# Kernel tuning notes

Measured on AMD Instinct MI355X. Metric: run time of the kernel, lower is better.

Reference implementation:

```python
import jax, jax.numpy as jnp
import numpy as np

N_HEADS = 16
D_MODEL = 1024
HEAD_DIM = D_MODEL // N_HEADS
B, S = 2, 2048


def setup_inputs() -> dict:
    key = jax.random.key(0)
    ks = jax.random.split(key, 10)
    scale = 1.0 / np.sqrt(D_MODEL)
    inp = {
        "query_tokens": jax.random.normal(ks[0], (B, S, D_MODEL), dtype=jnp.float32),
        "key_or_value_tokens": jax.random.normal(ks[1], (B, S, D_MODEL), dtype=jnp.float32),
        "mask": jnp.ones((B, S, S), dtype=jnp.int32),
        "Wq": jax.random.normal(ks[2], (D_MODEL, D_MODEL), dtype=jnp.float32) * scale,
        "bq": jnp.zeros((D_MODEL,), dtype=jnp.float32),
        "Wk": jax.random.normal(ks[3], (D_MODEL, D_MODEL), dtype=jnp.float32) * scale,
        "bk": jnp.zeros((D_MODEL,), dtype=jnp.float32),
        "Wv": jax.random.normal(ks[4], (D_MODEL, D_MODEL), dtype=jnp.float32) * scale,
        "bv": jnp.zeros((D_MODEL,), dtype=jnp.float32),
        "Wo": jax.random.normal(ks[5], (D_MODEL, D_MODEL), dtype=jnp.float32) * scale,
        "bo": jnp.zeros((D_MODEL,), dtype=jnp.float32),
    }
    return inp


def reference(query_tokens, key_or_value_tokens, mask, Wq, bq, Wk, bk, Wv, bv, Wo, bo):
    b, s, d = query_tokens.shape
    h, dh = N_HEADS, HEAD_DIM

    def proj(x, W, bias):
        # torch Linear: x @ W.T + b ; then split heads -> (b, h, s, dh)
        y = jnp.einsum("bsd,ed->bse", x, W) + bias
        return y.reshape(b, -1, h, dh).transpose(0, 2, 1, 3)

    q = proj(query_tokens, Wq, bq)
    k = proj(key_or_value_tokens, Wk, bk)
    v = proj(key_or_value_tokens, Wv, bv)

    scores = jnp.einsum("bhqd,bhkd->bhqk", q, k) / jnp.sqrt(jnp.float32(dh))
    # mask: (b, Sq, Sk) -> (b, 1, Sq, Sk); zeros get large negative fill
    scores = jnp.where(mask[:, None, :, :] == 0, jnp.float32(-1e9), scores)
    attn = jax.nn.softmax(scores, axis=-1)
    out = jnp.einsum("bhqk,bhkd->bhqd", attn, v)
    out = out.transpose(0, 2, 1, 3).reshape(b, s, d)
    return jnp.einsum("bsd,ed->bse", out, Wo) + bo
```

## Files before the change

### kernel.cpp

```cpp
#include <hip/hip_runtime.h>
#include <hip/hip_bf16.h>

typedef __bf16 bf16_8  __attribute__((ext_vector_type(8)));
typedef __bf16 bf16_4  __attribute__((ext_vector_type(4)));
typedef float  f32_4   __attribute__((ext_vector_type(4)));

#define NH 16
#define DHD 64
#define BB 2
#define SS 2048
#define DD 1024

__device__ __forceinline__ void gload16(const __bf16* g, __bf16* l) {
    __builtin_amdgcn_global_load_lds(
        (const __attribute__((address_space(1))) void*)g,
        (__attribute__((address_space(3))) void*)l, 16, 0, 0);
}

__global__ __launch_bounds__(256) void conv_mask(
    const float* __restrict__ s0, const float* __restrict__ s1,
    const float* __restrict__ s2, const float* __restrict__ s3,
    const float* __restrict__ s4, const float* __restrict__ s5,
    __bf16* __restrict__ d0, __bf16* __restrict__ d1, __bf16* __restrict__ d2,
    __bf16* __restrict__ d3, __bf16* __restrict__ d4, __bf16* __restrict__ d5,
    const int* __restrict__ mask, int* __restrict__ flags) {
    const int y = blockIdx.y;
    if (y >= 6) {
        if (blockIdx.x >= 1024) return;
        const int id = (y - 6) * 1024 + blockIdx.x;
        const int b = id >> 10, qt = (id >> 5) & 31, kt = id & 31;
        const int t = threadIdx.x;
        const int row = t >> 2, seg = t & 3;
        const int* p = mask + ((size_t)b * SS + qt * 64 + row) * SS + kt * 64 + seg * 16;
        int any0 = 0;
#pragma unroll
        for (int i = 0; i < 4; ++i) {
            int4 v = *(const int4*)&p[i * 4];
            any0 |= (v.x == 0) | (v.y == 0) | (v.z == 0) | (v.w == 0);
        }
        unsigned long long bal = __ballot(any0);
        __shared__ int sf[4];
        if ((t & 63) == 0) sf[t >> 6] = (bal != 0ULL);
        __syncthreads();
        if (t == 0) flags[id] = sf[0] | sf[1] | sf[2] | sf[3];
        return;
    }
    if (y >= 2 && blockIdx.x >= 1024) return;
    const float* s = (y == 0) ? s0 : (y == 1) ? s1 : (y == 2) ? s2
                   : (y == 3) ? s3 : (y == 4) ? s4 : s5;
    __bf16* d      = (y == 0) ? d0 : (y == 1) ? d1 : (y == 2) ? d2
                   : (y == 3) ? d3 : (y == 4) ? d4 : d5;
    const int i = (blockIdx.x * 256 + threadIdx.x) * 4;
    f32_4 v = *(const f32_4*)&s[i];
    bf16_4 o; o[0] = (__bf16)v[0]; o[1] = (__bf16)v[1];
    o[2] = (__bf16)v[2]; o[3] = (__bf16)v[3];
    *(bf16_4*)&d[i] = o;
}

template <int LAYOUT>
__device__ __forceinline__ void gemm_body(const __bf16* __restrict__ A,
                                          const __bf16* __restrict__ W,
                                          const float* __restrict__ bias,
                                          __bf16* __restrict__ out,
                                          __bf16* smem, int m0, int n0) {
    __bf16* ldsA0 = smem;
    __bf16* ldsB0 = smem + 4096;
    __bf16* ldsA1 = smem + 6144;
    __bf16* ldsB1 = smem + 10240;
    __bf16* ldsC  = smem;

    const int tid  = threadIdx.x;
    const int lane = tid & 63;
    const int w    = tid >> 6;
    const int quad = lane >> 4;
    const int l15  = lane & 15;
    const int wm   = w * 32;

    f32_4 acc[2][4] = {};

#define QSTAGE(KT, LA, LB)                                                     \
    do {                                                                       \
        _Pragma("unroll") for (int cc = 0; cc < 2; ++cc) {                     \
            const int c   = tid + cc * 256;                                    \
            const int row = c >> 2;                                            \
            const int cp  = c & 3;                                             \
            gload16(&A[(size_t)(m0 + row) * 1024 + (KT) + cp * 8],             \
                    &(LA)[c * 8]);                                             \
        }                                                                      \
        {                                                                      \
            const int c   = tid;                                               \
            const int row = c >> 2;                                            \
            const int cp  = c & 3;                                             \
            gload16(&W[(size_t)(n0 + row) * 1024 + (KT) + cp * 8],             \
                    &(LB)[c * 8]);                                             \
        }                                                                      \
    } while (0)

    QSTAGE(0, ldsA0, ldsB0);
    __syncthreads();

    for (int kt = 0; kt < 1024; kt += 32) {
        const int sel = (kt >> 5) & 1;
        const __bf16* la = sel ? ldsA1 : ldsA0;
        const __bf16* lb = sel ? ldsB1 : ldsB0;
        __bf16* na       = sel ? ldsA0 : ldsA1;
        __bf16* nb       = sel ? ldsB0 : ldsB1;
        if (kt + 32 < 1024) QSTAGE(kt + 32, na, nb);

        bf16_8 af[2], bfr[4];
#pragma unroll
        for (int i = 0; i < 2; ++i)
            af[i] = *(const bf16_8*)&la[(wm + i * 16 + l15) * 32 + quad * 8];
#pragma unroll
        for (int j = 0; j < 4; ++j)
            bfr[j] = *(const bf16_8*)&lb[(j * 16 + l15) * 32 + quad * 8];
#pragma unroll
        for (int i = 0; i < 2; ++i)
#pragma unroll
            for (int j = 0; j < 4; ++j)
                acc[i][j] = __builtin_amdgcn_mfma_f32_16x16x32_bf16(
                    af[i], bfr[j], acc[i][j], 0, 0, 0);

        __syncthreads();
    }
#undef QSTAGE

    if (LAYOUT == 2) {
#pragma unroll
        for (int i = 0; i < 2; ++i)
#pragma unroll
            for (int j = 0; j < 4; ++j) {
                const int col = n0 + j * 16 + l15;
                const float bv = bias[col];
                bf16_4 pk;
#pragma unroll
                for (int r = 0; r < 4; ++r) pk[r] = (__bf16)(acc[i][j][r] + bv);
                *(bf16_4*)&ldsC[(j * 16 + l15) * 136 + wm + i * 16 + quad * 4] = pk;
            }
        __syncthreads();
#pragma unroll
        for (int it = 0; it < 4; ++it) {
            const int g    = it * 256 + tid;
            const int colp = g >> 4;
            const int s8   = (g & 15) * 8;
            bf16_8 v = *(const bf16_8*)&ldsC[colp * 136 + s8];
            const int gcol = n0 + colp;
            const int grow = m0 + s8;
            *(bf16_8*)&out[(((size_t)(grow >> 11) * NH + (gcol >> 6)) * DHD +
                            (gcol & 63)) * SS + (grow & 2047)] = v;
        }
    } else {
#pragma unroll
        for (int i = 0; i < 2; ++i)
#pragma unroll
            for (int j = 0; j < 4; ++j) {
                const int col = n0 + j * 16 + l15;
                const float bv = bias[col];
#pragma unroll
                for (int r = 0; r < 4; ++r)
                    ldsC[(wm + i * 16 + quad * 4 + r) * 72 + j * 16 + l15] =
                        (__bf16)(acc[i][j][r] + bv);
            }
        __syncthreads();
#pragma unroll
        for (int it = 0; it < 4; ++it) {
            const int g   = it * 256 + tid;
            const int row = g >> 3;
            const int c8  = (g & 7) * 8;
            bf16_8 v = *(const bf16_8*)&ldsC[row * 72 + c8];
            const int grow = m0 + row;
            const int gcol = n0 + c8;
            *(bf16_8*)&out[(((size_t)(grow >> 11) * NH + (gcol >> 6)) * SS +
                            (grow & 2047)) * DHD + (gcol & 63)] = v;
        }
    }
}

__global__ __launch_bounds__(256) void gemm_qkv(
    const __bf16* __restrict__ Xq, const __bf16* __restrict__ Xkv,
    const __bf16* __restrict__ Wq, const float* __restrict__ bq,
    const __bf16* __restrict__ Wk, const float* __restrict__ bk,
    const __bf16* __restrict__ Wv, const float* __restrict__ bv,
    __bf16* __restrict__ Qo, __bf16* __restrict__ Ko, __bf16* __restrict__ VTo) {
    __shared__ __align__(16) __bf16 smem[12288];
    const int p  = blockIdx.x + 32 * (blockIdx.y + 16 * blockIdx.z);
    const int l  = (p & 7) * 192 + (p >> 3);
    const int xm = l & 31;
    const int yn = (l >> 5) & 15;
    const int z  = l >> 9;
    const __bf16* A    = (z == 0) ? Xq : Xkv;
    const __bf16* W    = (z == 0) ? Wq : (z == 1 ? Wk : Wv);
    const float* bias  = (z == 0) ? bq : (z == 1 ? bk : bv);
    if (z == 2)
        gemm_body<2>(A, W, bias, VTo, smem, xm * 128, yn * 64);
    else
        gemm_body<0>(A, W, bias, (z == 0) ? Qo : Ko, smem, xm * 128, yn * 64);
}

__global__ __launch_bounds__(256) void gemm_final(
    const __bf16* __restrict__ A, const __bf16* __restrict__ W,
    const float* __restrict__ bias, float* __restrict__ out) {
    __shared__ __align__(16) float smemf[128 * 68];
    __bf16* ldsA0 = (__bf16*)smemf;
    __bf16* ldsB0 = (__bf16*)smemf + 4096;
    __bf16* ldsA1 = (__bf16*)smemf + 6144;
    __bf16* ldsB1 = (__bf16*)smemf + 10240;
    float*  ldsC  = smemf;

    const int tid  = threadIdx.x;
    const int lane = tid & 63;
    const int w    = tid >> 6;
    const int quad = lane >> 4;
    const int l15  = lane & 15;
    const int wm   = w * 32;
    const int p   = blockIdx.x + 32 * blockIdx.y;
    const int lg  = (p & 7) * 64 + (p >> 3);
    const int m0  = (lg & 31) * 128;
    const int n0  = (lg >> 5) * 64;

    f32_4 acc[2][4] = {};

#define FSTAGE(KT, LA, LB)                                                     \
    do {                                                                       \
        _Pragma("unroll") for (int cc = 0; cc < 2; ++cc) {                     \
            const int c   = tid + cc * 256;                                    \
            const int row = c >> 2;                                            \
            const int cp  = c & 3;                                             \
            gload16(&A[(size_t)(m0 + row) * 1024 + (KT) + cp * 8],             \
                    &(LA)[c * 8]);                                             \
        }                                                                      \
        {                                                                      \
            const int c   = tid;                                               \
            const int row = c >> 2;                                            \
            const int cp  = c & 3;                                             \
            gload16(&W[(size_t)(n0 + row) * 1024 + (KT) + cp * 8],             \
                    &(LB)[c * 8]);                                             \
        }                                                                      \
    } while (0)

    FSTAGE(0, ldsA0, ldsB0);
    __syncthreads();

    for (int kt = 0; kt < 1024; kt += 32) {
        const int sel = (kt >> 5) & 1;
        const __bf16* la = sel ? ldsA1 : ldsA0;
        const __bf16* lb = sel ? ldsB1 : ldsB0;
        __bf16* na       = sel ? ldsA0 : ldsA1;
        __bf16* nb       = sel ? ldsB0 : ldsB1;
        if (kt + 32 < 1024) FSTAGE(kt + 32, na, nb);

        bf16_8 af[2], bfr[4];
#pragma unroll
        for (int i = 0; i < 2; ++i)
            af[i] = *(const bf16_8*)&la[(wm + i * 16 + l15) * 32 + quad * 8];
#pragma unroll
        for (int j = 0; j < 4; ++j)
            bfr[j] = *(const bf16_8*)&lb[(j * 16 + l15) * 32 + quad * 8];
#pragma unroll
        for (int i = 0; i < 2; ++i)
#pragma unroll
            for (int j = 0; j < 4; ++j)
                acc[i][j] = __builtin_amdgcn_mfma_f32_16x16x32_bf16(
                    af[i], bfr[j], acc[i][j], 0, 0, 0);

        __syncthreads();
    }
#undef FSTAGE

#pragma unroll
    for (int i = 0; i < 2; ++i)
#pragma unroll
        for (int j = 0; j < 4; ++j) {
            const int col = n0 + j * 16 + l15;
            const float bv = bias[col];
#pragma unroll
            for (int r = 0; r < 4; ++r)
                ldsC[(wm + i * 16 + quad * 4 + r) * 68 + j * 16 + l15] =
                    acc[i][j][r] + bv;
        }
    __syncthreads();
#pragma unroll
    for (int it = 0; it < 8; ++it) {
        const int g   = it * 256 + tid;
        const int row = g >> 4;
        const int c4  = (g & 15) * 4;
        f32_4 v = *(const f32_4*)&ldsC[row * 68 + c4];
        *(f32_4*)&out[(size_t)(m0 + row) * 1024 + n0 + c4] = v;
    }
}

__global__ __launch_bounds__(256, 2) void flash_attn(
    const __bf16* __restrict__ Q, const __bf16* __restrict__ K,
    const __bf16* __restrict__ VT, const int* __restrict__ mask,
    const int* __restrict__ flags, __bf16* __restrict__ O) {
    __shared__ __align__(16) __bf16 ldsK0[64 * 64];
    __shared__ __align__(16) __bf16 ldsK1[64 * 64];
    __shared__ __align__(16) __bf16 ldsV0[64 * 64];
    __shared__ __align__(16) __bf16 ldsV1[64 * 64];
    __shared__ __align__(16) __bf16 ldsP0[128 * 72];
    __shared__ __align__(16) __bf16 ldsP1[128 * 72];

    const int tid  = threadIdx.x;
    const int lane = tid & 63;
    const int w    = tid >> 6;
    const int quad = lane >> 4;
    const int l15  = lane & 15;
    const int p   = blockIdx.x + 16 * blockIdx.y;
    const int lg  = (p & 7) * 64 + (p >> 3);
    const int qx  = lg & 15;
    const int bh  = lg >> 4;
    const int q0  = qx * 128;
    const int b   = bh >> 4;

    const __bf16* Qb  = Q + (size_t)bh * SS * DHD;
    const __bf16* Kb  = K + (size_t)bh * SS * DHD;
    const __bf16* VTb = VT + (size_t)bh * DHD * SS;
    const int*    mb  = mask + (size_t)b * SS * SS;
    const int*    flb = flags + (size_t)b * 1024 + qx * 64;

    bf16_8 qa[2][2];
#pragma unroll
    for (int mt = 0; mt < 2; ++mt)
#pragma unroll
        for (int ks = 0; ks < 2; ++ks) {
            bf16_8 t = *(const bf16_8*)&Qb[(size_t)(q0 + w * 32 + mt * 16 + l15) * DHD +
                                           ks * 32 + quad * 8];
#pragma unroll
            for (int e = 0; e < 8; ++e)
                qa[mt][ks][e] = (__bf16)((float)t[e] * 0.18033688011112042f);
        }

    bf16_8 ones;
#pragma unroll
    for (int e = 0; e < 8; ++e) ones[e] = (__bf16)1.0f;

    f32_4 of[2][4] = {};
    f32_4 lsum[2] = {};

    const int c0 = tid, c1 = tid + 256;
    const int r_0 = c0 >> 3, r_1 = c1 >> 3;
    const int s_0 = (c0 & 7) ^ (r_0 & 7);
    const int s_1 = (c1 & 7) ^ (r_1 & 7);

#define STAGE_K(K0_, DST)                                                      \
    do {                                                                       \
        gload16(&Kb[(size_t)((K0_) + r_0) * DHD + s_0 * 8], &(DST)[c0 * 8]);   \
        gload16(&Kb[(size_t)((K0_) + r_1) * DHD + s_1 * 8], &(DST)[c1 * 8]);   \
    } while (0)
#define STAGE_V(K0_, DST)                                                      \
    do {                                                                       \
        gload16(&VTb[(size_t)r_0 * SS + (K0_) + s_0 * 8], &(DST)[c0 * 8]);     \
        gload16(&VTb[(size_t)r_1 * SS + (K0_) + s_1 * 8], &(DST)[c1 * 8]);     \
    } while (0)

    const int xq = l15 & 7;

#define QKT(KSRC, SA)                                                          \
    do {                                                                       \
        _Pragma("unroll") for (int ks = 0; ks < 2; ++ks) {                     \
            bf16_8 kb[4];                                                      \
            _Pragma("unroll") for (int j = 0; j < 4; ++j)                      \
                kb[j] = *(const bf16_8*)&(KSRC)[(j * 16 + l15) * 64 +          \
                                                (((ks * 4 + quad) ^ xq) * 8)]; \
            _Pragma("unroll") for (int mt = 0; mt < 2; ++mt)                   \
                _Pragma("unroll") for (int j = 0; j < 4; ++j)                  \
                    SA[mt][j] = __builtin_amdgcn_mfma_f32_16x16x32_bf16(       \
                        kb[j], qa[mt][ks], SA[mt][j], 0, 0, 0);                \
        }                                                                      \
    } while (0)

#define MASKF(TN, SA)                                                          \
    do {                                                                       \
        if ((flb[TN] | flb[32 + (TN)]) != 0) {                                 \
            _Pragma("unroll") for (int mt = 0; mt < 2; ++mt)                   \
                _Pragma("unroll") for (int j = 0; j < 4; ++j)                  \
                    _Pragma("unroll") for (int r = 0; r < 4; ++r) {            \
                        const int qg = q0 + w * 32 + mt * 16 + l15;            \
                        const int kg = (TN) * 64 + j * 16 + quad * 4 + r;      \
                        if (mb[(size_t)qg * SS + kg] == 0) SA[mt][j][r] = -1e9f; \
                    }                                                          \
        }                                                                      \
    } while (0)

#define EXPW(SA, PDST)                                                         \
    do {                                                                       \
        _Pragma("unroll") for (int mt = 0; mt < 2; ++mt)                       \
            _Pragma("unroll") for (int j = 0; j < 4; ++j) {                    \
                bf16_4 pk;                                                     \
                _Pragma("unroll") for (int r = 0; r < 4; ++r)                  \
                    pk[r] = (__bf16)__builtin_amdgcn_exp2f(SA[mt][j][r]);      \
                *(bf16_4*)&(PDST)[(w * 32 + mt * 16 + l15) * 72 + j * 16 +     \
                                  quad * 4] = pk;                              \
            }                                                                  \
    } while (0)

#define PV(VSRC, PSRC)                                                         \
    do {                                                                       \
        _Pragma("unroll") for (int ks2 = 0; ks2 < 2; ++ks2) {                  \
            bf16_8 pa[2], vb[4];                                               \
            _Pragma("unroll") for (int mt = 0; mt < 2; ++mt)                   \
                pa[mt] = *(const bf16_8*)&(PSRC)[(w * 32 + mt * 16 + l15) * 72 \
                                                 + ks2 * 32 + quad * 8];       \
            _Pragma("unroll") for (int jo = 0; jo < 4; ++jo)                   \
                vb[jo] = *(const bf16_8*)&(VSRC)[(jo * 16 + l15) * 64 +        \
                                                 (((ks2 * 4 + quad) ^ xq) * 8)]; \
            __builtin_amdgcn_s_setprio(1);                                     \
            _Pragma("unroll") for (int mt = 0; mt < 2; ++mt) {                 \
                _Pragma("unroll") for (int jo = 0; jo < 4; ++jo)               \
                    of[mt][jo] = __builtin_amdgcn_mfma_f32_16x16x32_bf16(      \
                        pa[mt], vb[jo], of[mt][jo], 0, 0, 0);                  \
                lsum[mt] = __builtin_amdgcn_mfma_f32_16x16x32_bf16(            \
                    pa[mt], ones, lsum[mt], 0, 0, 0);                          \
            }                                                                  \
            __builtin_amdgcn_s_setprio(0);                                     \
        }                                                                      \
    } while (0)

    STAGE_K(0, ldsK0);
    STAGE_V(0, ldsV0);
    __syncthreads();
    STAGE_K(64, ldsK1);
    STAGE_V(64, ldsV1);
    {
        f32_4 sa[2][4] = {};
        QKT(ldsK0, sa);
        MASKF(0, sa);
        EXPW(sa, ldsP0);
    }
    __syncthreads();

    for (int t = 0; t < 31; ++t) {
        const int sel = t & 1;
        __bf16* kst       = sel ? ldsK1 : ldsK0;
        const __bf16* kn  = sel ? ldsK0 : ldsK1;
        const __bf16* vc  = sel ? ldsV1 : ldsV0;
        const __bf16* pc  = sel ? ldsP1 : ldsP0;
        __bf16* pn        = sel ? ldsP0 : ldsP1;
        __bf16* vst       = sel ? ldsV1 : ldsV0;

        if (t < 30) STAGE_K((t + 2) * 64, kst);

        f32_4 sa[2][4] = {};
        QKT(kn, sa);
        MASKF(t + 1, sa);
        PV(vc, pc);
        EXPW(sa, pn);

        __syncthreads();
        if (t < 30) STAGE_V((t + 2) * 64, vst);
    }

    PV(ldsV1, ldsP1);

    const int hcol = (bh & 15) * 64;
#pragma unroll
    for (int mt = 0; mt < 2; ++mt)
#pragma unroll
        for (int r = 0; r < 4; ++r) {
            const float inv = 1.0f / fmaxf(lsum[mt][r], 1e-37f);
            const int qg = q0 + w * 32 + mt * 16 + quad * 4 + r;
#pragma unroll
            for (int jo = 0; jo < 4; ++jo)
                O[((size_t)b * SS + qg) * DD + hcol + jo * 16 + l15] =
                    (__bf16)(of[mt][jo][r] * inv);
        }
#undef STAGE_K
#undef STAGE_V
#undef QKT
#undef MASKF
#undef EXPW
#undef PV
}


extern "C" void kernel_launch(void* const* d_in, const int* in_sizes, int n_in,
                              void* d_out, int out_size, void* d_ws, size_t ws_size,
                              hipStream_t stream) {
    const float* xq   = (const float*)d_in[0];
    const float* xkv  = (const float*)d_in[1];
    const int*   mask = (const int*)d_in[2];
    const float* Wq   = (const float*)d_in[3];
    const float* bq   = (const float*)d_in[4];
    const float* Wk   = (const float*)d_in[5];
    const float* bk   = (const float*)d_in[6];
    const float* Wv   = (const float*)d_in[7];
    const float* bv   = (const float*)d_in[8];
    const float* Wo   = (const float*)d_in[9];
    const float* bo   = (const float*)d_in[10];

    __bf16* ws = (__bf16*)d_ws;
    const size_t big = (size_t)BB * SS * DD;
    const size_t wsz = (size_t)DD * DD;
    __bf16* Qw   = ws;
    __bf16* Kw   = Qw + big;
    __bf16* VTw  = Kw + big;
    __bf16* Aw   = VTw + big;
    __bf16* Xqb  = Aw + big;
    __bf16* Xkvb = Xqb + big;
    __bf16* Wqb  = Xkvb + big;
    __bf16* Wkb  = Wqb + wsz;
    __bf16* Wvb  = Wkb + wsz;
    __bf16* Wob  = Wvb + wsz;
    int* flags   = (int*)(Wob + wsz);

    conv_mask<<<dim3(4096, 8), dim3(256), 0, stream>>>(xq, xkv, Wq, Wk, Wv, Wo,
                                                       Xqb, Xkvb, Wqb, Wkb, Wvb, Wob,
                                                       mask, flags);
    gemm_qkv<<<dim3(32, 16, 3), dim3(256), 0, stream>>>(Xqb, Xkvb, Wqb, bq, Wkb, bk,
                                                        Wvb, bv, Qw, Kw, VTw);
    flash_attn<<<dim3(SS / 128, BB * NH), dim3(256), 0, stream>>>(Qw, Kw, VTw, mask,
                                                                  flags, Aw);
    gemm_final<<<dim3(32, 16), dim3(256), 0, stream>>>(Aw, Wob, bo, (float*)d_out);
}
```

Before: 231.8 us.

## Shrink flash-attention query tile to 64 rows and drop GEMM block swizzles

The flash-attention kernel now handles 64 query rows per block (16 per wave) instead of 128. It also collapses the two P staging buffers into one per-wave-private buffer and raises the launch bound to 3 blocks per CU. This doubles the grid and cuts per-block register and LDS use, aiming for more occupancy and parallelism, at the cost of loading K/V tiles twice as often. The XCD-aware block index remapping in both GEMM kernels is replaced with direct blockIdx mapping, which may change L2 locality across dies.

```diff
diff --git a/kernel.cpp b/kernel.cpp
--- a/kernel.cpp
+++ b/kernel.cpp
@@ -183,18 +183,15 @@
     const __bf16* __restrict__ Wv, const float* __restrict__ bv,
     __bf16* __restrict__ Qo, __bf16* __restrict__ Ko, __bf16* __restrict__ VTo) {
     __shared__ __align__(16) __bf16 smem[12288];
-    const int p  = blockIdx.x + 32 * (blockIdx.y + 16 * blockIdx.z);
-    const int l  = (p & 7) * 192 + (p >> 3);
-    const int xm = l & 31;
-    const int yn = (l >> 5) & 15;
-    const int z  = l >> 9;
+    const int z = blockIdx.z;
     const __bf16* A    = (z == 0) ? Xq : Xkv;
     const __bf16* W    = (z == 0) ? Wq : (z == 1 ? Wk : Wv);
     const float* bias  = (z == 0) ? bq : (z == 1 ? bk : bv);
     if (z == 2)
-        gemm_body<2>(A, W, bias, VTo, smem, xm * 128, yn * 64);
+        gemm_body<2>(A, W, bias, VTo, smem, blockIdx.x * 128, blockIdx.y * 64);
     else
-        gemm_body<0>(A, W, bias, (z == 0) ? Qo : Ko, smem, xm * 128, yn * 64);
+        gemm_body<0>(A, W, bias, (z == 0) ? Qo : Ko, smem,
+                     blockIdx.x * 128, blockIdx.y * 64);
 }
 
 __global__ __launch_bounds__(256) void gemm_final(
@@ -213,10 +210,8 @@
     const int quad = lane >> 4;
     const int l15  = lane & 15;
     const int wm   = w * 32;
-    const int p   = blockIdx.x + 32 * blockIdx.y;
-    const int lg  = (p & 7) * 64 + (p >> 3);
-    const int m0  = (lg & 31) * 128;
-    const int n0  = (lg >> 5) * 64;
+    const int m0   = blockIdx.x * 128;
+    const int n0   = blockIdx.y * 64;
 
     f32_4 acc[2][4] = {};
 
@@ -289,7 +284,7 @@
     }
 }
 
-__global__ __launch_bounds__(256, 2) void flash_attn(
+__global__ __launch_bounds__(256, 3) void flash_attn(
     const __bf16* __restrict__ Q, const __bf16* __restrict__ K,
     const __bf16* __restrict__ VT, const int* __restrict__ mask,
     const int* __restrict__ flags, __bf16* __restrict__ O) {
@@ -297,45 +292,42 @@
     __shared__ __align__(16) __bf16 ldsK1[64 * 64];
     __shared__ __align__(16) __bf16 ldsV0[64 * 64];
     __shared__ __align__(16) __bf16 ldsV1[64 * 64];
-    __shared__ __align__(16) __bf16 ldsP0[128 * 72];
-    __shared__ __align__(16) __bf16 ldsP1[128 * 72];
+    __shared__ __align__(16) __bf16 ldsP[64 * 68];
 
     const int tid  = threadIdx.x;
     const int lane = tid & 63;
     const int w    = tid >> 6;
     const int quad = lane >> 4;
     const int l15  = lane & 15;
-    const int p   = blockIdx.x + 16 * blockIdx.y;
-    const int lg  = (p & 7) * 64 + (p >> 3);
-    const int qx  = lg & 15;
-    const int bh  = lg >> 4;
-    const int q0  = qx * 128;
+    const int p   = blockIdx.x + 32 * blockIdx.y;
+    const int lg  = (p & 7) * 128 + (p >> 3);
+    const int qx  = lg & 31;
+    const int bh  = lg >> 5;
+    const int q0  = qx * 64;
     const int b   = bh >> 4;
 
     const __bf16* Qb  = Q + (size_t)bh * SS * DHD;
     const __bf16* Kb  = K + (size_t)bh * SS * DHD;
     const __bf16* VTb = VT + (size_t)bh * DHD * SS;
     const int*    mb  = mask + (size_t)b * SS * SS;
-    const int*    flb = flags + (size_t)b * 1024 + qx * 64;
-
-    bf16_8 qa[2][2];
-#pragma unroll
-    for (int mt = 0; mt < 2; ++mt)
-#pragma unroll
-        for (int ks = 0; ks < 2; ++ks) {
-            bf16_8 t = *(const bf16_8*)&Qb[(size_t)(q0 + w * 32 + mt * 16 + l15) * DHD +
-                                           ks * 32 + quad * 8];
-#pragma unroll
-            for (int e = 0; e < 8; ++e)
-                qa[mt][ks][e] = (__bf16)((float)t[e] * 0.18033688011112042f);
-        }
+    const int*    flb = flags + (size_t)b * 1024 + qx * 32;
+
+    bf16_8 qa[2];
+#pragma unroll
+    for (int ks = 0; ks < 2; ++ks) {
+        bf16_8 t = *(const bf16_8*)&Qb[(size_t)(q0 + w * 16 + l15) * DHD +
+                                       ks * 32 + quad * 8];
+#pragma unroll
+        for (int e = 0; e < 8; ++e)
+            qa[ks][e] = (__bf16)((float)t[e] * 0.18033688011112042f);
+    }
 
     bf16_8 ones;
 #pragma unroll
     for (int e = 0; e < 8; ++e) ones[e] = (__bf16)1.0f;
 
-    f32_4 of[2][4] = {};
-    f32_4 lsum[2] = {};
+    f32_4 of[4] = {};
+    f32_4 lsum = {};
 
     const int c0 = tid, c1 = tid + 256;
     const int r_0 = c0 >> 3, r_1 = c1 >> 3;
@@ -362,56 +354,49 @@
             _Pragma("unroll") for (int j = 0; j < 4; ++j)                      \
                 kb[j] = *(const bf16_8*)&(KSRC)[(j * 16 + l15) * 64 +          \
                                                 (((ks * 4 + quad) ^ xq) * 8)]; \
-            _Pragma("unroll") for (int mt = 0; mt < 2; ++mt)                   \
-                _Pragma("unroll") for (int j = 0; j < 4; ++j)                  \
-                    SA[mt][j] = __builtin_amdgcn_mfma_f32_16x16x32_bf16(       \
-                        kb[j], qa[mt][ks], SA[mt][j], 0, 0, 0);                \
+            _Pragma("unroll") for (int j = 0; j < 4; ++j)                      \
+                SA[j] = __builtin_amdgcn_mfma_f32_16x16x32_bf16(               \
+                    kb[j], qa[ks], SA[j], 0, 0, 0);                            \
         }                                                                      \
     } while (0)
 
 #define MASKF(TN, SA)                                                          \
     do {                                                                       \
-        if ((flb[TN] | flb[32 + (TN)]) != 0) {                                 \
-            _Pragma("unroll") for (int mt = 0; mt < 2; ++mt)                   \
-                _Pragma("unroll") for (int j = 0; j < 4; ++j)                  \
-                    _Pragma("unroll") for (int r = 0; r < 4; ++r) {            \
-                        const int qg = q0 + w * 32 + mt * 16 + l15;            \
-                        const int kg = (TN) * 64 + j * 16 + quad * 4 + r;      \
-                        if (mb[(size_t)qg * SS + kg] == 0) SA[mt][j][r] = -1e9f; \
-                    }                                                          \
-        }                                                                      \
-    } while (0)
-
-#define EXPW(SA, PDST)                                                         \
-    do {                                                                       \
-        _Pragma("unroll") for (int mt = 0; mt < 2; ++mt)                       \
-            _Pragma("unroll") for (int j = 0; j < 4; ++j) {                    \
-                bf16_4 pk;                                                     \
-                _Pragma("unroll") for (int r = 0; r < 4; ++r)                  \
-                    pk[r] = (__bf16)__builtin_amdgcn_exp2f(SA[mt][j][r]);      \
-                *(bf16_4*)&(PDST)[(w * 32 + mt * 16 + l15) * 72 + j * 16 +     \
-                                  quad * 4] = pk;                              \
-            }                                                                  \
-    } while (0)
-
-#define PV(VSRC, PSRC)                                                         \
+        if (flb[TN] != 0) {                                                    \
+            _Pragma("unroll") for (int j = 0; j < 4; ++j)                      \
+                _Pragma("unroll") for (int r = 0; r < 4; ++r) {                \
+                    const int qg = q0 + w * 16 + l15;                          \
+                    const int kg = (TN) * 64 + j * 16 + quad * 4 + r;          \
+                    if (mb[(size_t)qg * SS + kg] == 0) SA[j][r] = -1e9f;       \
+                }                                                              \
+        }                                                                      \
+    } while (0)
+
+#define EXPW(SA)                                                               \
+    do {                                                                       \
+        _Pragma("unroll") for (int j = 0; j < 4; ++j) {                        \
+            bf16_4 pk;                                                         \
+            _Pragma("unroll") for (int r = 0; r < 4; ++r)                      \
+                pk[r] = (__bf16)__builtin_amdgcn_exp2f(SA[j][r]);              \
+            *(bf16_4*)&ldsP[(w * 16 + l15) * 68 + j * 16 + quad * 4] = pk;     \
+        }                                                                      \
+    } while (0)
+
+#define PV(VSRC)                                                               \
     do {                                                                       \
         _Pragma("unroll") for (int ks2 = 0; ks2 < 2; ++ks2) {                  \
-            bf16_8 pa[2], vb[4];                                               \
-            _Pragma("unroll") for (int mt = 0; mt < 2; ++mt)                   \
-                pa[mt] = *(const bf16_8*)&(PSRC)[(w * 32 + mt * 16 + l15) * 72 \
-                                                 + ks2 * 32 + quad * 8];       \
+            bf16_8 pa, vb[4];                                                  \
+            pa = *(const bf16_8*)&ldsP[(w * 16 + l15) * 68 + ks2 * 32 +        \
+                                       quad * 8];                              \
             _Pragma("unroll") for (int jo = 0; jo < 4; ++jo)                   \
                 vb[jo] = *(const bf16_8*)&(VSRC)[(jo * 16 + l15) * 64 +        \
                                                  (((ks2 * 4 + quad) ^ xq) * 8)]; \
             __builtin_amdgcn_s_setprio(1);                                     \
-            _Pragma("unroll") for (int mt = 0; mt < 2; ++mt) {                 \
-                _Pragma("unroll") for (int jo = 0; jo < 4; ++jo)               \
-                    of[mt][jo] = __builtin_amdgcn_mfma_f32_16x16x32_bf16(      \
-                        pa[mt], vb[jo], of[mt][jo], 0, 0, 0);                  \
-                lsum[mt] = __builtin_amdgcn_mfma_f32_16x16x32_bf16(            \
-                    pa[mt], ones, lsum[mt], 0, 0, 0);                          \
-            }                                                                  \
+            _Pragma("unroll") for (int jo = 0; jo < 4; ++jo)                   \
+                of[jo] = __builtin_amdgcn_mfma_f32_16x16x32_bf16(              \
+                    pa, vb[jo], of[jo], 0, 0, 0);                              \
+            lsum = __builtin_amdgcn_mfma_f32_16x16x32_bf16(                    \
+                pa, ones, lsum, 0, 0, 0);                                      \
             __builtin_amdgcn_s_setprio(0);                                     \
         }                                                                      \
     } while (0)
@@ -422,10 +407,10 @@
     STAGE_K(64, ldsK1);
     STAGE_V(64, ldsV1);
     {
-        f32_4 sa[2][4] = {};
+        f32_4 sa[4] = {};
         QKT(ldsK0, sa);
         MASKF(0, sa);
-        EXPW(sa, ldsP0);
+        EXPW(sa);
     }
     __syncthreads();
 
@@ -434,36 +419,32 @@
         __bf16* kst       = sel ? ldsK1 : ldsK0;
         const __bf16* kn  = sel ? ldsK0 : ldsK1;
         const __bf16* vc  = sel ? ldsV1 : ldsV0;
-        const __bf16* pc  = sel ? ldsP1 : ldsP0;
-        __bf16* pn        = sel ? ldsP0 : ldsP1;
         __bf16* vst       = sel ? ldsV1 : ldsV0;
 
         if (t < 30) STAGE_K((t + 2) * 64, kst);
 
-        f32_4 sa[2][4] = {};
+        f32_4 sa[4] = {};
         QKT(kn, sa);
         MASKF(t + 1, sa);
-        PV(vc, pc);
-        EXPW(sa, pn);
+        PV(vc);
+        EXPW(sa);
 
         __syncthreads();
         if (t < 30) STAGE_V((t + 2) * 64, vst);
     }
 
-    PV(ldsV1, ldsP1);
+    PV(ldsV1);
 
     const int hcol = (bh & 15) * 64;
 #pragma unroll
-    for (int mt = 0; mt < 2; ++mt)
-#pragma unroll
-        for (int r = 0; r < 4; ++r) {
-            const float inv = 1.0f / fmaxf(lsum[mt][r], 1e-37f);
-            const int qg = q0 + w * 32 + mt * 16 + quad * 4 + r;
-#pragma unroll
-            for (int jo = 0; jo < 4; ++jo)
-                O[((size_t)b * SS + qg) * DD + hcol + jo * 16 + l15] =
-                    (__bf16)(of[mt][jo][r] * inv);
-        }
+    for (int r = 0; r < 4; ++r) {
+        const float inv = 1.0f / fmaxf(lsum[r], 1e-37f);
+        const int qg = q0 + w * 16 + quad * 4 + r;
+#pragma unroll
+        for (int jo = 0; jo < 4; ++jo)
+            O[((size_t)b * SS + qg) * DD + hcol + jo * 16 + l15] =
+                (__bf16)(of[jo][r] * inv);
+    }
 #undef STAGE_K
 #undef STAGE_V
 #undef QKT
@@ -508,7 +489,7 @@
                                                        mask, flags);
     gemm_qkv<<<dim3(32, 16, 3), dim3(256), 0, stream>>>(Xqb, Xkvb, Wqb, bq, Wkb, bk,
                                                         Wvb, bv, Qw, Kw, VTw);
-    flash_attn<<<dim3(SS / 128, BB * NH), dim3(256), 0, stream>>>(Qw, Kw, VTw, mask,
-                                                                  flags, Aw);
+    flash_attn<<<dim3(32, 32), dim3(256), 0, stream>>>(Qw, Kw, VTw, mask,
+                                                       flags, Aw);
     gemm_final<<<dim3(32, 16), dim3(256), 0, stream>>>(Aw, Wob, bo, (float*)d_out);
 }
```

New measurement: 244.6 us. 5.5% more time.
